# Performance work log

Measured on AMD Instinct MI355X. Metric: run time of the kernel, lower is better.

The kernel has to match this reference:

```python
import jax, jax.numpy as jnp
import numpy as np

B, T, IN_F, F = 128, 256, 256, 256
TAU_MEM = 0.02
THRESH = 0.5
RESET = 0.0
BETA = 4.0
LN_EPS = 1e-6

# Fast-sigmoid surrogate spike: forward = Heaviside, backward = 1/(1+beta|x|)^2
@jax.custom_vjp
def spike_surrogate(x):
    return (x > 0.0).astype(x.dtype)

def _sp_fwd(x):
    return spike_surrogate(x), x

def _sp_bwd(x, g):
    return (g / jnp.square(1.0 + BETA * jnp.abs(x)),)

spike_surrogate.defvjp(_sp_fwd, _sp_bwd)


def setup_inputs() -> dict:
    key = jax.random.key(0)
    k0, k1 = jax.random.split(key)
    spikes = jax.random.uniform(k0, (B, T, IN_F), dtype=jnp.float32)
    W = jax.random.normal(k1, (IN_F, F), dtype=jnp.float32) / np.sqrt(IN_F)
    b = jnp.zeros((F,), jnp.float32)
    ln_scale = jnp.ones((T, F), jnp.float32)   # distinct LayerNorm per timestep
    ln_bias = jnp.zeros((T, F), jnp.float32)
    return {"spikes": spikes, "W": W, "b": b, "ln_scale": ln_scale, "ln_bias": ln_bias}


def reference(spikes, W, b, ln_scale, ln_bias):
    # Dense is shared across timesteps -> one big contraction, same math.
    currents = jnp.einsum('bti,if->btf', spikes, W) + b  # [B,T,F]
    alpha = jnp.exp(jnp.asarray(-1.0 / TAU_MEM, spikes.dtype))

    def step(v_mem, xs):
        cur, gamma, beta_ln = xs  # [B,F], [F], [F]
        v_mem = alpha * v_mem + (1.0 - alpha) * cur
        s = spike_surrogate(v_mem - THRESH)
        v_mem = v_mem * (1.0 - s) + RESET * s
        mu = jnp.mean(s, axis=-1, keepdims=True)
        var = jnp.var(s, axis=-1, keepdims=True)
        y = (s - mu) * jax.lax.rsqrt(var + LN_EPS) * gamma + beta_ln
        return v_mem, y

    v0 = jnp.zeros((spikes.shape[0], W.shape[1]), spikes.dtype)
    xs = (jnp.swapaxes(currents, 0, 1), ln_scale, ln_bias)  # time-major
    _, ys = jax.lax.scan(step, v0, xs)  # ys: [T,B,F]
    return jnp.swapaxes(ys, 0, 1)  # [B,T,F]
```

## Files before the change

### kernel.cpp

```cpp
#include <hip/hip_runtime.h>
#include <math.h>

#define NROWS 32768
#define NK 256
#define NF 256
#define NT_SEQ 256
#define MTILE 32
#define TAU 5e-4f


typedef __attribute__((ext_vector_type(4))) float f32x4;
typedef __attribute__((ext_vector_type(8))) _Float16 f16x8;

__device__ __forceinline__ unsigned short f16_bits(float x) {
    return __builtin_bit_cast(unsigned short, (_Float16)x);
}

__global__ void split_w(const float* __restrict__ W, unsigned short* __restrict__ wt) {
    const int k = blockIdx.x;
    const int col = threadIdx.x;
    const float w16 = W[k * NF + col] * 16.0f;
    const _Float16 h1 = (_Float16)w16;
    const float r = (w16 - (float)h1) * 2048.0f;
    const _Float16 h2 = (_Float16)r;
    const int ks = k >> 5, chunk = (k >> 3) & 3, j = k & 7;
    const int base = ((ks * 4 + chunk) * 2048) + col * 8 + j;
    wt[base] = __builtin_bit_cast(unsigned short, h1);
    wt[base + 65536] = __builtin_bit_cast(unsigned short, h2);
}

__global__ __launch_bounds__(512)
void lif_main(const float* __restrict__ spikes,
              const float* __restrict__ W,
              const float* __restrict__ bias,
              const float* __restrict__ ln_scale,
              const float* __restrict__ ln_bias,
              const unsigned short* __restrict__ wt,
              float* __restrict__ out)
{
    __shared__ __align__(16) short alds[2][MTILE][264];
    __shared__ unsigned int bits[MTILE][8];
    __shared__ float rinv_s[MTILE], mu_s[MTILE];
    __shared__ unsigned int elist[64];
    __shared__ int ecnt;

    const int tid = threadIdx.x;
    const int lane = tid & 63;
    const int wid = tid >> 6;
    const int row0 = blockIdx.x * MTILE;

    if (tid == 0) ecnt = 0;

    #pragma unroll
    for (int it = 0; it < 4; ++it) {
        const int idx = it * 2048 + tid * 4;
        const int r = idx >> 8, c = idx & 255;
        const float4 v = *reinterpret_cast<const float4*>(
            spikes + (size_t)(row0 + r) * NK + c);
        unsigned short h[4], l[4];
        const float fv[4] = {v.x, v.y, v.z, v.w};
        #pragma unroll
        for (int e = 0; e < 4; ++e) {
            h[e] = f16_bits(fv[e]);
            const float hf = (float)__builtin_bit_cast(_Float16, h[e]);
            l[e] = f16_bits((fv[e] - hf) * 2048.0f);
        }
        *(uint2*)&alds[0][r][c] = make_uint2((unsigned int)h[0] | ((unsigned int)h[1] << 16),
                                             (unsigned int)h[2] | ((unsigned int)h[3] << 16));
        *(uint2*)&alds[1][r][c] = make_uint2((unsigned int)l[0] | ((unsigned int)l[1] << 16),
                                             (unsigned int)l[2] | ((unsigned int)l[3] << 16));
    }
    __syncthreads();

    f32x4 acc0[2][2], acc1[2][2];
    {
        const f32x4 z = {0.f, 0.f, 0.f, 0.f};
        #pragma unroll
        for (int mt = 0; mt < 2; ++mt)
            #pragma unroll
            for (int nt = 0; nt < 2; ++nt) { acc0[mt][nt] = z; acc1[mt][nt] = z; }
    }
    const int a_off = (lane & 15) * 264 + (lane >> 4) * 8;
    const int b_off = (lane >> 4) * 2048 + (wid * 32 + (lane & 15)) * 8;
    const short* alds_flat = &alds[0][0][0];

    for (int ks = 0; ks < 8; ++ks) {
        f16x8 bf[2][2];
        #pragma unroll
        for (int c = 0; c < 2; ++c)
            #pragma unroll
            for (int nt = 0; nt < 2; ++nt)
                bf[c][nt] = *reinterpret_cast<const f16x8*>(
                    wt + c * 65536 + ks * 8192 + b_off + nt * 128);
        f16x8 ah[2], al[2];
        #pragma unroll
        for (int mt = 0; mt < 2; ++mt) {
            ah[mt] = *reinterpret_cast<const f16x8*>(
                alds_flat + (mt * 16) * 264 + ks * 32 + a_off);
            al[mt] = *reinterpret_cast<const f16x8*>(
                alds_flat + 8448 + (mt * 16) * 264 + ks * 32 + a_off);
        }
        #pragma unroll
        for (int mt = 0; mt < 2; ++mt)
            #pragma unroll
            for (int nt = 0; nt < 2; ++nt) {
                acc0[mt][nt] = __builtin_amdgcn_mfma_f32_16x16x32_f16(ah[mt], bf[0][nt], acc0[mt][nt], 0, 0, 0);
                acc1[mt][nt] = __builtin_amdgcn_mfma_f32_16x16x32_f16(ah[mt], bf[1][nt], acc1[mt][nt], 0, 0, 0);
                acc1[mt][nt] = __builtin_amdgcn_mfma_f32_16x16x32_f16(al[mt], bf[0][nt], acc1[mt][nt], 0, 0, 0);
            }
    }

    unsigned int smask[2] = {0u, 0u};
    #pragma unroll
    for (int mt = 0; mt < 2; ++mt)
        #pragma unroll
        for (int nt = 0; nt < 2; ++nt) {
            const int gcol = wid * 32 + nt * 16 + (lane & 15);
            const float bv = bias[gcol];
            #pragma unroll
            for (int reg = 0; reg < 4; ++reg) {
                const float v = fmaf(acc1[mt][nt][reg], 4.8828125e-4f,
                                     acc0[mt][nt][reg]) * 0.0625f + bv;
                if ((v - 0.5f) > 0.0f) smask[mt] |= 1u << (nt * 4 + reg);
                if (__builtin_expect(fabsf(v - 0.5f) < TAU, 0)) {
                    const int rl = mt * 16 + (lane >> 4) * 4 + reg;
                    const int ei = atomicAdd(&ecnt, 1);
                    if (ei < 64) elist[ei] = (unsigned int)((rl << 8) | gcol);
                }
            }
        }

    #pragma unroll
    for (int mt = 0; mt < 2; ++mt)
        #pragma unroll
        for (int reg = 0; reg < 4; ++reg) {
            const unsigned long long m0 = __ballot((smask[mt] >> (reg)) & 1u);
            const unsigned long long m1 = __ballot((smask[mt] >> (4 + reg)) & 1u);
            if (lane < 4) {
                const int g = lane;
                const unsigned int w =
                    (unsigned int)((m0 >> (g * 16)) & 0xFFFFull) |
                    ((unsigned int)((m1 >> (g * 16)) & 0xFFFFull) << 16);
                bits[mt * 16 + g * 4 + reg][wid] = w;
            }
        }
    __syncthreads();

    const int ne = min(ecnt, 64);
    for (int e = wid; e < ne; e += 8) {
        const unsigned int pk = elist[e];
        const int rl = (int)(pk >> 8), gcol = (int)(pk & 255u);
        const float* sr = spikes + (size_t)(row0 + rl) * NK;
        const float* wc = W + gcol;
        const int k0 = lane * 4;
        const double p0 = (double)sr[k0 + 0] * (double)wc[(size_t)(k0 + 0) * NF];
        const double p1 = (double)sr[k0 + 1] * (double)wc[(size_t)(k0 + 1) * NF];
        const double p2 = (double)sr[k0 + 2] * (double)wc[(size_t)(k0 + 2) * NF];
        const double p3 = (double)sr[k0 + 3] * (double)wc[(size_t)(k0 + 3) * NF];
        double pl = (p0 + p1) + (p2 + p3);
        #pragma unroll
        for (int off = 32; off > 0; off >>= 1) pl += __shfl_down(pl, off);
        if (lane == 0) {
            const double vex = pl + (double)bias[gcol];
            const bool sex = (vex - 0.5) > 0.0;
            const bool spv = (bits[rl][gcol >> 5] >> (gcol & 31)) & 1u;
            if (sex != spv) atomicXor(&bits[rl][gcol >> 5], 1u << (gcol & 31));
        }
    }
    __syncthreads();

    if (tid < MTILE) {
        int kc = 0;
        #pragma unroll
        for (int w = 0; w < 8; ++w) kc += __popc(bits[tid][w]);
        const double mu = (double)kc * (1.0 / 256.0);
        const double var = mu * (1.0 - mu);
        rinv_s[tid] = (float)(1.0 / sqrt(var + 1e-6));
        mu_s[tid] = (float)mu;
    }
    __syncthreads();

    const int orow = tid >> 4;
    const int of0 = (tid & 15) * 4;
    const int grow = row0 + orow;
    const int t = grow & (NT_SEQ - 1);
    const float rinv = rinv_s[orow];
    const float muf = mu_s[orow];
    #pragma unroll
    for (int j = 0; j < 4; ++j) {
        const int f = of0 + j * 64;
        const unsigned int wb = bits[orow][f >> 5];
        const int sh = f & 31;
        const float4 g4 = *reinterpret_cast<const float4*>(&ln_scale[t * NF + f]);
        const float4 b4 = *reinterpret_cast<const float4*>(&ln_bias[t * NF + f]);
        float4 o;
        const float s0 = ((wb >> (sh + 0)) & 1u) ? 1.0f : 0.0f;
        const float s1 = ((wb >> (sh + 1)) & 1u) ? 1.0f : 0.0f;
        const float s2 = ((wb >> (sh + 2)) & 1u) ? 1.0f : 0.0f;
        const float s3 = ((wb >> (sh + 3)) & 1u) ? 1.0f : 0.0f;
        o.x = (s0 - muf) * rinv * g4.x + b4.x;
        o.y = (s1 - muf) * rinv * g4.y + b4.y;
        o.z = (s2 - muf) * rinv * g4.z + b4.z;
        o.w = (s3 - muf) * rinv * g4.w + b4.w;
        *reinterpret_cast<float4*>(&out[(size_t)grow * NF + f]) = o;
    }
}

extern "C" void kernel_launch(void* const* d_in, const int* in_sizes, int n_in,
                              void* d_out, int out_size, void* d_ws, size_t ws_size,
                              hipStream_t stream) {
    const float* spikes   = (const float*)d_in[0];
    const float* W        = (const float*)d_in[1];
    const float* bias     = (const float*)d_in[2];
    const float* ln_scale = (const float*)d_in[3];
    const float* ln_bias  = (const float*)d_in[4];
    float* out = (float*)d_out;
    unsigned short* wt = (unsigned short*)d_ws;

    split_w<<<dim3(256), dim3(256), 0, stream>>>(W, wt);
    lif_main<<<dim3(NROWS / MTILE), dim3(512), 0, stream>>>(
        spikes, W, bias, ln_scale, ln_bias, wt, out);
}
```

Measured before the change: 40.35 us.

## Drop LDS staging of A tile and halve block to 256 threads

The spike tile is no longer staged and split into fp16 hi/lo in shared memory. Each wave now loads its A fragments straight from global memory and splits them in registers. The block shrinks to 4 waves, each covering 64 output columns, so every A fragment feeds more MFMAs. This removes the LDS fill, a barrier and the LDS footprint, which may raise occupancy. The cost is redundant global A loads across the 4 waves (served by cache), more accumulator registers, and the hi/lo conversion repeated per wave.

```diff
diff --git a/kernel.cpp b/kernel.cpp
--- a/kernel.cpp
+++ b/kernel.cpp
@@ -29,7 +29,7 @@
     wt[base + 65536] = __builtin_bit_cast(unsigned short, h2);
 }
 
-__global__ __launch_bounds__(512)
+__global__ __launch_bounds__(256, 3)
 void lif_main(const float* __restrict__ spikes,
               const float* __restrict__ W,
               const float* __restrict__ bias,
@@ -38,7 +38,6 @@
               const unsigned short* __restrict__ wt,
               float* __restrict__ out)
 {
-    __shared__ __align__(16) short alds[2][MTILE][264];
     __shared__ unsigned int bits[MTILE][8];
     __shared__ float rinv_s[MTILE], mu_s[MTILE];
     __shared__ unsigned int elist[64];
@@ -50,72 +49,57 @@
     const int row0 = blockIdx.x * MTILE;
 
     if (tid == 0) ecnt = 0;
-
-    #pragma unroll
-    for (int it = 0; it < 4; ++it) {
-        const int idx = it * 2048 + tid * 4;
-        const int r = idx >> 8, c = idx & 255;
-        const float4 v = *reinterpret_cast<const float4*>(
-            spikes + (size_t)(row0 + r) * NK + c);
-        unsigned short h[4], l[4];
-        const float fv[4] = {v.x, v.y, v.z, v.w};
-        #pragma unroll
-        for (int e = 0; e < 4; ++e) {
-            h[e] = f16_bits(fv[e]);
-            const float hf = (float)__builtin_bit_cast(_Float16, h[e]);
-            l[e] = f16_bits((fv[e] - hf) * 2048.0f);
-        }
-        *(uint2*)&alds[0][r][c] = make_uint2((unsigned int)h[0] | ((unsigned int)h[1] << 16),
-                                             (unsigned int)h[2] | ((unsigned int)h[3] << 16));
-        *(uint2*)&alds[1][r][c] = make_uint2((unsigned int)l[0] | ((unsigned int)l[1] << 16),
-                                             (unsigned int)l[2] | ((unsigned int)l[3] << 16));
-    }
-    __syncthreads();
-
-    f32x4 acc0[2][2], acc1[2][2];
+    __syncthreads();
+
+    const float* a_base = spikes + (size_t)(row0 + (lane & 15)) * NK + (lane >> 4) * 8;
+    const int b_base = (lane >> 4) * 2048 + (wid * 64 + (lane & 15)) * 8;
+
+    f32x4 acc0[2][4], acc1[2][4];
     {
         const f32x4 z = {0.f, 0.f, 0.f, 0.f};
         #pragma unroll
         for (int mt = 0; mt < 2; ++mt)
             #pragma unroll
-            for (int nt = 0; nt < 2; ++nt) { acc0[mt][nt] = z; acc1[mt][nt] = z; }
-    }
-    const int a_off = (lane & 15) * 264 + (lane >> 4) * 8;
-    const int b_off = (lane >> 4) * 2048 + (wid * 32 + (lane & 15)) * 8;
-    const short* alds_flat = &alds[0][0][0];
-
+            for (int nt = 0; nt < 4; ++nt) { acc0[mt][nt] = z; acc1[mt][nt] = z; }
+    }
+
+    #pragma unroll 2
     for (int ks = 0; ks < 8; ++ks) {
-        f16x8 bf[2][2];
-        #pragma unroll
-        for (int c = 0; c < 2; ++c)
-            #pragma unroll
-            for (int nt = 0; nt < 2; ++nt)
-                bf[c][nt] = *reinterpret_cast<const f16x8*>(
-                    wt + c * 65536 + ks * 8192 + b_off + nt * 128);
         f16x8 ah[2], al[2];
         #pragma unroll
         for (int mt = 0; mt < 2; ++mt) {
-            ah[mt] = *reinterpret_cast<const f16x8*>(
-                alds_flat + (mt * 16) * 264 + ks * 32 + a_off);
-            al[mt] = *reinterpret_cast<const f16x8*>(
-                alds_flat + 8448 + (mt * 16) * 264 + ks * 32 + a_off);
-        }
-        #pragma unroll
-        for (int mt = 0; mt < 2; ++mt)
-            #pragma unroll
-            for (int nt = 0; nt < 2; ++nt) {
-                acc0[mt][nt] = __builtin_amdgcn_mfma_f32_16x16x32_f16(ah[mt], bf[0][nt], acc0[mt][nt], 0, 0, 0);
-                acc1[mt][nt] = __builtin_amdgcn_mfma_f32_16x16x32_f16(ah[mt], bf[1][nt], acc1[mt][nt], 0, 0, 0);
-                acc1[mt][nt] = __builtin_amdgcn_mfma_f32_16x16x32_f16(al[mt], bf[0][nt], acc1[mt][nt], 0, 0, 0);
-            }
+            const float* p = a_base + (size_t)(mt * 16) * NK + ks * 32;
+            const float4 u = *reinterpret_cast<const float4*>(p);
+            const float4 v = *reinterpret_cast<const float4*>(p + 4);
+            const float fv[8] = {u.x, u.y, u.z, u.w, v.x, v.y, v.z, v.w};
+            #pragma unroll
+            for (int e = 0; e < 8; ++e) {
+                const _Float16 h = (_Float16)fv[e];
+                ah[mt][e] = h;
+                al[mt][e] = (_Float16)((fv[e] - (float)h) * 2048.0f);
+            }
+        }
+        #pragma unroll
+        for (int nt = 0; nt < 4; ++nt) {
+            const f16x8 b1 = *reinterpret_cast<const f16x8*>(
+                wt + ks * 8192 + b_base + nt * 128);
+            const f16x8 b2 = *reinterpret_cast<const f16x8*>(
+                wt + 65536 + ks * 8192 + b_base + nt * 128);
+            #pragma unroll
+            for (int mt = 0; mt < 2; ++mt) {
+                acc0[mt][nt] = __builtin_amdgcn_mfma_f32_16x16x32_f16(ah[mt], b1, acc0[mt][nt], 0, 0, 0);
+                acc1[mt][nt] = __builtin_amdgcn_mfma_f32_16x16x32_f16(ah[mt], b2, acc1[mt][nt], 0, 0, 0);
+                acc1[mt][nt] = __builtin_amdgcn_mfma_f32_16x16x32_f16(al[mt], b1, acc1[mt][nt], 0, 0, 0);
+            }
+        }
     }
 
     unsigned int smask[2] = {0u, 0u};
     #pragma unroll
     for (int mt = 0; mt < 2; ++mt)
         #pragma unroll
-        for (int nt = 0; nt < 2; ++nt) {
-            const int gcol = wid * 32 + nt * 16 + (lane & 15);
+        for (int nt = 0; nt < 4; ++nt) {
+            const int gcol = wid * 64 + nt * 16 + (lane & 15);
             const float bv = bias[gcol];
             #pragma unroll
             for (int reg = 0; reg < 4; ++reg) {
@@ -134,20 +118,27 @@
     for (int mt = 0; mt < 2; ++mt)
         #pragma unroll
         for (int reg = 0; reg < 4; ++reg) {
-            const unsigned long long m0 = __ballot((smask[mt] >> (reg)) & 1u);
-            const unsigned long long m1 = __ballot((smask[mt] >> (4 + reg)) & 1u);
+            unsigned long long m[4];
+            #pragma unroll
+            for (int nt = 0; nt < 4; ++nt)
+                m[nt] = __ballot((smask[mt] >> (nt * 4 + reg)) & 1u);
             if (lane < 4) {
                 const int g = lane;
-                const unsigned int w =
-                    (unsigned int)((m0 >> (g * 16)) & 0xFFFFull) |
-                    ((unsigned int)((m1 >> (g * 16)) & 0xFFFFull) << 16);
-                bits[mt * 16 + g * 4 + reg][wid] = w;
+                const unsigned int w0 =
+                    (unsigned int)((m[0] >> (g * 16)) & 0xFFFFull) |
+                    ((unsigned int)((m[1] >> (g * 16)) & 0xFFFFull) << 16);
+                const unsigned int w1 =
+                    (unsigned int)((m[2] >> (g * 16)) & 0xFFFFull) |
+                    ((unsigned int)((m[3] >> (g * 16)) & 0xFFFFull) << 16);
+                const int rl = mt * 16 + g * 4 + reg;
+                bits[rl][wid * 2 + 0] = w0;
+                bits[rl][wid * 2 + 1] = w1;
             }
         }
     __syncthreads();
 
     const int ne = min(ecnt, 64);
-    for (int e = wid; e < ne; e += 8) {
+    for (int e = wid; e < ne; e += 4) {
         const unsigned int pk = elist[e];
         const int rl = (int)(pk >> 8), gcol = (int)(pk & 255u);
         const float* sr = spikes + (size_t)(row0 + rl) * NK;
@@ -180,17 +171,17 @@
     }
     __syncthreads();
 
-    const int orow = tid >> 4;
-    const int of0 = (tid & 15) * 4;
+    const int orow = tid >> 3;
+    const int of0 = (tid & 7) * 4;
     const int grow = row0 + orow;
     const int t = grow & (NT_SEQ - 1);
     const float rinv = rinv_s[orow];
     const float muf = mu_s[orow];
     #pragma unroll
-    for (int j = 0; j < 4; ++j) {
-        const int f = of0 + j * 64;
-        const unsigned int wb = bits[orow][f >> 5];
-        const int sh = f & 31;
+    for (int j = 0; j < 8; ++j) {
+        const int f = of0 + j * 32;
+        const unsigned int wb = bits[orow][j];
+        const int sh = of0;
         const float4 g4 = *reinterpret_cast<const float4*>(&ln_scale[t * NF + f]);
         const float4 b4 = *reinterpret_cast<const float4*>(&ln_bias[t * NF + f]);
         float4 o;
@@ -218,6 +209,6 @@
     unsigned short* wt = (unsigned short*)d_ws;
 
     split_w<<<dim3(256), dim3(256), 0, stream>>>(W, wt);
-    lif_main<<<dim3(NROWS / MTILE), dim3(512), 0, stream>>>(
+    lif_main<<<dim3(NROWS / MTILE), dim3(256), 0, stream>>>(
         spikes, W, bias, ln_scale, ln_bias, wt, out);
 }
```

Result: slower. 64.27 us (+59.3%).

## Replace split-fp16 GEMM with single bf16 MFMA plus wider fp64 fix-up band

Applied to the files above, without the earlier changes.

Drops the two-term fp16 splitting of both spikes and W (three MFMAs per tile) and uses one bf16 MFMA per tile, halving LDS staging and weight traffic. The larger rounding error is covered by widening the near-threshold band that gets an exact fp64 recompute, with the exception list grown to 256 entries. It also sets a launch-bounds occupancy hint. The risk is more fp64 fix-up work, and overflow of the list in blocks with many near-threshold values, which would give wrong spikes.

```diff
diff --git a/kernel.cpp b/kernel.cpp
--- a/kernel.cpp
+++ b/kernel.cpp
@@ -6,30 +6,26 @@
 #define NF 256
 #define NT_SEQ 256
 #define MTILE 32
-#define TAU 5e-4f
+#define TAU 8e-3f
 
 
 typedef __attribute__((ext_vector_type(4))) float f32x4;
-typedef __attribute__((ext_vector_type(8))) _Float16 f16x8;
+typedef __attribute__((ext_vector_type(8))) short bf16x8;
 
-__device__ __forceinline__ unsigned short f16_bits(float x) {
-    return __builtin_bit_cast(unsigned short, (_Float16)x);
+__device__ __forceinline__ unsigned short bf16_rne(float f) {
+    unsigned int u = __builtin_bit_cast(unsigned int, f);
+    u += 0x7FFFu + ((u >> 16) & 1u);
+    return (unsigned short)(u >> 16);
 }
 
 __global__ void split_w(const float* __restrict__ W, unsigned short* __restrict__ wt) {
     const int k = blockIdx.x;
     const int col = threadIdx.x;
-    const float w16 = W[k * NF + col] * 16.0f;
-    const _Float16 h1 = (_Float16)w16;
-    const float r = (w16 - (float)h1) * 2048.0f;
-    const _Float16 h2 = (_Float16)r;
     const int ks = k >> 5, chunk = (k >> 3) & 3, j = k & 7;
-    const int base = ((ks * 4 + chunk) * 2048) + col * 8 + j;
-    wt[base] = __builtin_bit_cast(unsigned short, h1);
-    wt[base + 65536] = __builtin_bit_cast(unsigned short, h2);
+    wt[(ks * 4 + chunk) * 2048 + col * 8 + j] = bf16_rne(W[k * NF + col]);
 }
 
-__global__ __launch_bounds__(512)
+__global__ __launch_bounds__(512, 6)
 void lif_main(const float* __restrict__ spikes,
               const float* __restrict__ W,
               const float* __restrict__ bias,
@@ -38,10 +34,10 @@
               const unsigned short* __restrict__ wt,
               float* __restrict__ out)
 {
-    __shared__ __align__(16) short alds[2][MTILE][264];
+    __shared__ __align__(16) short alds[MTILE][264];
     __shared__ unsigned int bits[MTILE][8];
     __shared__ float rinv_s[MTILE], mu_s[MTILE];
-    __shared__ unsigned int elist[64];
+    __shared__ unsigned int elist[256];
     __shared__ int ecnt;
 
     const int tid = threadIdx.x;
@@ -52,62 +48,39 @@
     if (tid == 0) ecnt = 0;
 
     #pragma unroll
-    for (int it = 0; it < 4; ++it) {
-        const int idx = it * 2048 + tid * 4;
-        const int r = idx >> 8, c = idx & 255;
-        const float4 v = *reinterpret_cast<const float4*>(
-            spikes + (size_t)(row0 + r) * NK + c);
-        unsigned short h[4], l[4];
-        const float fv[4] = {v.x, v.y, v.z, v.w};
-        #pragma unroll
-        for (int e = 0; e < 4; ++e) {
-            h[e] = f16_bits(fv[e]);
-            const float hf = (float)__builtin_bit_cast(_Float16, h[e]);
-            l[e] = f16_bits((fv[e] - hf) * 2048.0f);
-        }
-        *(uint2*)&alds[0][r][c] = make_uint2((unsigned int)h[0] | ((unsigned int)h[1] << 16),
-                                             (unsigned int)h[2] | ((unsigned int)h[3] << 16));
-        *(uint2*)&alds[1][r][c] = make_uint2((unsigned int)l[0] | ((unsigned int)l[1] << 16),
-                                             (unsigned int)l[2] | ((unsigned int)l[3] << 16));
+    for (int it = 0; it < 2; ++it) {
+        const int idx = it * 512 + tid;
+        const int r = idx >> 5, c8 = (idx & 31) * 8;
+        const float* p = spikes + (size_t)(row0 + r) * NK + c8;
+        const float4 u = *reinterpret_cast<const float4*>(p);
+        const float4 v = *reinterpret_cast<const float4*>(p + 4);
+        const unsigned int w0 = (unsigned int)bf16_rne(u.x) | ((unsigned int)bf16_rne(u.y) << 16);
+        const unsigned int w1 = (unsigned int)bf16_rne(u.z) | ((unsigned int)bf16_rne(u.w) << 16);
+        const unsigned int w2 = (unsigned int)bf16_rne(v.x) | ((unsigned int)bf16_rne(v.y) << 16);
+        const unsigned int w3 = (unsigned int)bf16_rne(v.z) | ((unsigned int)bf16_rne(v.w) << 16);
+        *reinterpret_cast<uint4*>(&alds[r][c8]) = make_uint4(w0, w1, w2, w3);
     }
     __syncthreads();
 
-    f32x4 acc0[2][2], acc1[2][2];
+    f32x4 acc[2][2];
     {
         const f32x4 z = {0.f, 0.f, 0.f, 0.f};
-        #pragma unroll
-        for (int mt = 0; mt < 2; ++mt)
-            #pragma unroll
-            for (int nt = 0; nt < 2; ++nt) { acc0[mt][nt] = z; acc1[mt][nt] = z; }
+        acc[0][0] = z; acc[0][1] = z; acc[1][0] = z; acc[1][1] = z;
     }
     const int a_off = (lane & 15) * 264 + (lane >> 4) * 8;
-    const int b_off = (lane >> 4) * 2048 + (wid * 32 + (lane & 15)) * 8;
-    const short* alds_flat = &alds[0][0][0];
+    const int b_base = (lane >> 4) * 2048 + (wid * 32 + (lane & 15)) * 8;
+    const short* alds_flat = &alds[0][0];
 
+    #pragma unroll 2
     for (int ks = 0; ks < 8; ++ks) {
-        f16x8 bf[2][2];
-        #pragma unroll
-        for (int c = 0; c < 2; ++c)
-            #pragma unroll
-            for (int nt = 0; nt < 2; ++nt)
-                bf[c][nt] = *reinterpret_cast<const f16x8*>(
-                    wt + c * 65536 + ks * 8192 + b_off + nt * 128);
-        f16x8 ah[2], al[2];
-        #pragma unroll
-        for (int mt = 0; mt < 2; ++mt) {
-            ah[mt] = *reinterpret_cast<const f16x8*>(
-                alds_flat + (mt * 16) * 264 + ks * 32 + a_off);
-            al[mt] = *reinterpret_cast<const f16x8*>(
-                alds_flat + 8448 + (mt * 16) * 264 + ks * 32 + a_off);
-        }
-        #pragma unroll
-        for (int mt = 0; mt < 2; ++mt)
-            #pragma unroll
-            for (int nt = 0; nt < 2; ++nt) {
-                acc0[mt][nt] = __builtin_amdgcn_mfma_f32_16x16x32_f16(ah[mt], bf[0][nt], acc0[mt][nt], 0, 0, 0);
-                acc1[mt][nt] = __builtin_amdgcn_mfma_f32_16x16x32_f16(ah[mt], bf[1][nt], acc1[mt][nt], 0, 0, 0);
-                acc1[mt][nt] = __builtin_amdgcn_mfma_f32_16x16x32_f16(al[mt], bf[0][nt], acc1[mt][nt], 0, 0, 0);
-            }
+        const bf16x8 b0 = *reinterpret_cast<const bf16x8*>(wt + ks * 8192 + b_base);
+        const bf16x8 b1 = *reinterpret_cast<const bf16x8*>(wt + ks * 8192 + b_base + 128);
+        const bf16x8 a0 = *reinterpret_cast<const bf16x8*>(alds_flat + ks * 32 + a_off);
+        const bf16x8 a1 = *reinterpret_cast<const bf16x8*>(alds_flat + 16 * 264 + ks * 32 + a_off);
+        acc[0][0] = __builtin_amdgcn_mfma_f32_16x16x32_bf16(a0, b0, acc[0][0], 0, 0, 0);
+        acc[0][1] = __builtin_amdgcn_mfma_f32_16x16x32_bf16(a0, b1, acc[0][1], 0, 0, 0);
+        acc[1][0] = __builtin_amdgcn_mfma_f32_16x16x32_bf16(a1, b0, acc[1][0], 0, 0, 0);
+        acc[1][1] = __builtin_amdgcn_mfma_f32_16x16x32_bf16(a1, b1, acc[1][1], 0, 0, 0);
     }
 
     unsigned int smask[2] = {0u, 0u};
@@ -119,13 +92,12 @@
             const float bv = bias[gcol];
             #pragma unroll
             for (int reg = 0; reg < 4; ++reg) {
-                const float v = fmaf(acc1[mt][nt][reg], 4.8828125e-4f,
-                                     acc0[mt][nt][reg]) * 0.0625f + bv;
+                const float v = acc[mt][nt][reg] + bv;
                 if ((v - 0.5f) > 0.0f) smask[mt] |= 1u << (nt * 4 + reg);
                 if (__builtin_expect(fabsf(v - 0.5f) < TAU, 0)) {
                     const int rl = mt * 16 + (lane >> 4) * 4 + reg;
                     const int ei = atomicAdd(&ecnt, 1);
-                    if (ei < 64) elist[ei] = (unsigned int)((rl << 8) | gcol);
+                    if (ei < 256) elist[ei] = (unsigned int)((rl << 8) | gcol);
                 }
             }
         }
@@ -146,7 +118,7 @@
         }
     __syncthreads();
 
-    const int ne = min(ecnt, 64);
+    const int ne = min(ecnt, 256);
     for (int e = wid; e < ne; e += 8) {
         const unsigned int pk = elist[e];
         const int rl = (int)(pk >> 8), gcol = (int)(pk & 255u);
```

Measured after the change: 90.45 us. +124.1%, slower.
